# Performance work log

Measured on AMD Instinct MI355X. Metric: run time of the kernel, lower is better.

The kernel has to match this reference:

```python
import jax, jax.numpy as jnp
import numpy as np

CUT_DIST = 4.0            # cut_dist_bohr
FEATURES = 20
EPSILON = 1e-11
BOHR = 0.5291772105638411  # distance_mul (ase.units.Bohr)
POS_SCALE = 2.5


def setup_inputs() -> dict:
    key = jax.random.key(0)
    k1, k2 = jax.random.split(key)
    source = jax.random.normal(k1, (1, 4096, 3), dtype=jnp.float32) * POS_SCALE
    target = jax.random.normal(k2, (1, 2048, 3), dtype=jnp.float32) * POS_SCALE
    return {"source": source, "target": target}


def reference(source, target):
    # Pairwise diff between every source (probe) and target (atom): [B, N, M, 3]
    diff = target[:, None, :, :] - source[:, :, None, :]
    dist = jnp.sqrt(jnp.sum(diff * diff, axis=-1))            # [B, N, M]
    mask = dist < CUT_DIST                                    # [B, N, M] bool (self_send=True keeps d==0)
    direction = diff / (dist[..., None] + EPSILON)            # [B, N, M, 3]
    # sinc radial basis expansion on distances converted with distance_mul (Bohr)
    d = dist * BOHR + EPSILON                                 # [B, N, M]
    n = jnp.arange(1, FEATURES + 1, dtype=d.dtype)            # [F]
    d_exp = d[..., None]                                      # [B, N, M, 1]
    expansion = jnp.sin(n * jnp.pi * d_exp / CUT_DIST) / d_exp  # [B, N, M, F]
    return dist, direction, mask, expansion
```

## Files before the change

### kernel.cpp

```cpp
#include <hip/hip_runtime.h>
#include <math.h>

typedef float v4f __attribute__((ext_vector_type(4)));

#define CUT  4.0f
#define EPS  1e-11f
#define BOHR 0.5291772105638411f
#define PI_F 3.14159265358979323846f

#define LDS_FLOATS 18432

__device__ __forceinline__ float bperm(unsigned int lane, float v) {
    return __int_as_float(
        __builtin_amdgcn_ds_bpermute((int)(lane << 2), __float_as_int(v)));
}

__global__ __launch_bounds__(256) void deepdft_staged_kernel(
    const float* __restrict__ src,
    const float* __restrict__ tgt,
    float* __restrict__ out,
    unsigned int N, unsigned int M)
{
    __shared__ __align__(16) float lds[LDS_FLOATS];
    float* lsrc = lds;
    float* ltgt = lds + 3u * N;

    const unsigned int total = N * M;
    const unsigned int tid   = threadIdx.x;

    {
        const unsigned int ns = 3u * N;
        if ((ns & 3u) == 0u) {
            const unsigned int ns4 = ns >> 2;
            for (unsigned int i = tid; i < ns4; i += blockDim.x)
                ((v4f*)lsrc)[i] = ((const v4f*)src)[i];
        } else {
            for (unsigned int i = tid; i < ns; i += blockDim.x) lsrc[i] = src[i];
        }
        const unsigned int nt = 3u * M;
        if ((ns & 3u) == 0u && (nt & 3u) == 0u) {
            const unsigned int nt4 = nt >> 2;
            for (unsigned int i = tid; i < nt4; i += blockDim.x)
                ((v4f*)ltgt)[i] = ((const v4f*)tgt)[i];
        } else {
            for (unsigned int i = tid; i < nt; i += blockDim.x) ltgt[i] = tgt[i];
        }
    }
    __syncthreads();

    float* __restrict__ dist_o = out;
    float* __restrict__ dir_o  = out + (size_t)total;
    float* __restrict__ mask_o = out + (size_t)4 * total;
    float* __restrict__ exp_o  = out + (size_t)5 * total;

    const unsigned int lane   = tid & 63u;
    const unsigned int waves  = (gridDim.x * blockDim.x) >> 6;
    const unsigned int wtiles = (total + 63u) >> 6;

    for (unsigned int w = (blockIdx.x * blockDim.x + tid) >> 6;
         w < wtiles; w += waves) {
        const unsigned int base = w << 6;
        const unsigned int idx  = base + lane;
        const unsigned int cidx = (idx < total) ? idx : (total - 1u);

        unsigned int n = cidx / M;
        unsigned int m = cidx - n * M;

        float sx = lsrc[3u*n + 0], sy = lsrc[3u*n + 1], sz = lsrc[3u*n + 2];
        float tx = ltgt[3u*m + 0], ty = ltgt[3u*m + 1], tz = ltgt[3u*m + 2];

        float dx = tx - sx, dy = ty - sy, dz = tz - sz;
        float d2   = fmaf(dx, dx, fmaf(dy, dy, dz * dz));
        float dist = sqrtf(d2);
        float inv  = 1.0f / (dist + EPS);

        if (idx < total) {
            dist_o[idx] = dist;
            mask_o[idx] = (dist < CUT) ? 1.0f : 0.0f;
        }

        float ux = dx * inv, uy = dy * inv, uz = dz * inv;
        float d    = fmaf(dist, BOHR, EPS);
        float invd = 1.0f / d;
        float x    = (PI_F / CUT) * d;

        {
            float* gdir = dir_o + (size_t)3 * base;
            #pragma unroll
            for (int k = 0; k < 3; ++k) {
                unsigned int e = lane + 64u * (unsigned)k;
                unsigned int p = (e * 10923u) >> 15;
                unsigned int c = e - 3u * p;
                float vx = bperm(p, ux);
                float vy = bperm(p, uy);
                float vz = bperm(p, uz);
                float val = (c == 0u) ? vx : ((c == 1u) ? vy : vz);
                if (base + p < total) gdir[e] = val;
            }
        }

        {
            v4f* gexp = reinterpret_cast<v4f*>(exp_o) + (size_t)5 * base;
            #pragma unroll
            for (int k = 0; k < 5; ++k) {
                unsigned int j = lane + 64u * (unsigned)k;
                unsigned int p = (j * 6554u) >> 15;
                unsigned int g = j - 5u * p;
                float xv = bperm(p, x);
                float iv = bperm(p, invd);
                float n0 = (float)(4u * g + 1u);
                v4f v;
                v.x = __sinf( n0         * xv) * iv;
                v.y = __sinf((n0 + 1.0f) * xv) * iv;
                v.z = __sinf((n0 + 2.0f) * xv) * iv;
                v.w = __sinf((n0 + 3.0f) * xv) * iv;
                if (base + p < total) gexp[j] = v;
            }
        }
    }
}

__global__ __launch_bounds__(256) void deepdft_global_kernel(
    const float* __restrict__ src,
    const float* __restrict__ tgt,
    float* __restrict__ out,
    unsigned int N, unsigned int M)
{
    const unsigned int total = N * M;
    float* __restrict__ dist_o = out;
    float* __restrict__ dir_o  = out + (size_t)total;
    float* __restrict__ mask_o = out + (size_t)4 * total;
    float* __restrict__ exp_o  = out + (size_t)5 * total;

    const unsigned int lane   = threadIdx.x & 63u;
    const unsigned int waves  = (gridDim.x * blockDim.x) >> 6;
    const unsigned int wtiles = (total + 63u) >> 6;

    for (unsigned int w = (blockIdx.x * blockDim.x + threadIdx.x) >> 6;
         w < wtiles; w += waves) {
        const unsigned int base = w << 6;
        const unsigned int idx  = base + lane;
        const unsigned int cidx = (idx < total) ? idx : (total - 1u);
        unsigned int n = cidx / M;
        unsigned int m = cidx - n * M;

        float sx = src[3u*n + 0], sy = src[3u*n + 1], sz = src[3u*n + 2];
        float tx = tgt[3u*m + 0], ty = tgt[3u*m + 1], tz = tgt[3u*m + 2];
        float dx = tx - sx, dy = ty - sy, dz = tz - sz;
        float dist = sqrtf(fmaf(dx, dx, fmaf(dy, dy, dz * dz)));
        float inv  = 1.0f / (dist + EPS);

        if (idx < total) {
            dist_o[idx] = dist;
            mask_o[idx] = (dist < CUT) ? 1.0f : 0.0f;
        }
        float ux = dx * inv, uy = dy * inv, uz = dz * inv;
        float d    = fmaf(dist, BOHR, EPS);
        float invd = 1.0f / d;
        float x    = (PI_F / CUT) * d;

        {
            float* gdir = dir_o + (size_t)3 * base;
            #pragma unroll
            for (int k = 0; k < 3; ++k) {
                unsigned int e = lane + 64u * (unsigned)k;
                unsigned int p = (e * 10923u) >> 15;
                unsigned int c = e - 3u * p;
                float vx = bperm(p, ux);
                float vy = bperm(p, uy);
                float vz = bperm(p, uz);
                float val = (c == 0u) ? vx : ((c == 1u) ? vy : vz);
                if (base + p < total) gdir[e] = val;
            }
        }
        {
            v4f* gexp = reinterpret_cast<v4f*>(exp_o) + (size_t)5 * base;
            #pragma unroll
            for (int k = 0; k < 5; ++k) {
                unsigned int j = lane + 64u * (unsigned)k;
                unsigned int p = (j * 6554u) >> 15;
                unsigned int g = j - 5u * p;
                float xv = bperm(p, x);
                float iv = bperm(p, invd);
                float n0 = (float)(4u * g + 1u);
                v4f v;
                v.x = __sinf( n0         * xv) * iv;
                v.y = __sinf((n0 + 1.0f) * xv) * iv;
                v.z = __sinf((n0 + 2.0f) * xv) * iv;
                v.w = __sinf((n0 + 3.0f) * xv) * iv;
                if (base + p < total) gexp[j] = v;
            }
        }
    }
}

extern "C" void kernel_launch(void* const* d_in, const int* in_sizes, int n_in,
                              void* d_out, int out_size, void* d_ws, size_t ws_size,
                              hipStream_t stream) {
    const float* src = (const float*)d_in[0];
    const float* tgt = (const float*)d_in[1];
    float* out = (float*)d_out;

    unsigned int N = (unsigned int)(in_sizes[0] / 3);
    unsigned int M = (unsigned int)(in_sizes[1] / 3);
    unsigned int total = N * M;

    const unsigned int block = 256;
    unsigned int wtiles = (total + 63u) >> 6;
    unsigned int blocks = (wtiles + (block / 64) - 1) / (block / 64);
    if (blocks > 2048u) blocks = 2048u;

    if (3u * (N + M) <= (unsigned)LDS_FLOATS) {
        deepdft_staged_kernel<<<blocks, block, 0, stream>>>(src, tgt, out, N, M);
    } else {
        deepdft_global_kernel<<<blocks, block, 0, stream>>>(src, tgt, out, N, M);
    }
}
```

Measured before the change: 160.1 us.

## Batch eight wave tiles per phase with contiguous chunking and fewer blocks

The LDS-staged kernel now gives each wave a contiguous chunk of tiles instead of a grid stride. It processes tiles in groups of eight: first it computes distances for all eight and keeps the per-tile values in registers, then it writes all directions, then all expansions. The grid is capped at 512 blocks instead of 2048, so each block loads the source and target arrays into LDS fewer times in total. The aim is more independent work per wave and more back-to-back stores, at the cost of higher register pressure and fewer resident waves to hide latency.

```diff
diff --git a/kernel.cpp b/kernel.cpp
--- a/kernel.cpp
+++ b/kernel.cpp
@@ -9,13 +9,14 @@
 #define PI_F 3.14159265358979323846f
 
 #define LDS_FLOATS 18432
+#define T 8
 
 __device__ __forceinline__ float bperm(unsigned int lane, float v) {
     return __int_as_float(
         __builtin_amdgcn_ds_bpermute((int)(lane << 2), __float_as_int(v)));
 }
 
-__global__ __launch_bounds__(256) void deepdft_staged_kernel(
+__global__ __launch_bounds__(256) void deepdft_phased_kernel(
     const float* __restrict__ src,
     const float* __restrict__ tgt,
     float* __restrict__ out,
@@ -30,19 +31,15 @@
 
     {
         const unsigned int ns = 3u * N;
-        if ((ns & 3u) == 0u) {
-            const unsigned int ns4 = ns >> 2;
+        const unsigned int nt = 3u * M;
+        if ((ns & 3u) == 0u && (nt & 3u) == 0u) {
+            const unsigned int ns4 = ns >> 2, nt4 = nt >> 2;
             for (unsigned int i = tid; i < ns4; i += blockDim.x)
                 ((v4f*)lsrc)[i] = ((const v4f*)src)[i];
-        } else {
-            for (unsigned int i = tid; i < ns; i += blockDim.x) lsrc[i] = src[i];
-        }
-        const unsigned int nt = 3u * M;
-        if ((ns & 3u) == 0u && (nt & 3u) == 0u) {
-            const unsigned int nt4 = nt >> 2;
             for (unsigned int i = tid; i < nt4; i += blockDim.x)
                 ((v4f*)ltgt)[i] = ((const v4f*)tgt)[i];
         } else {
+            for (unsigned int i = tid; i < ns; i += blockDim.x) lsrc[i] = src[i];
             for (unsigned int i = tid; i < nt; i += blockDim.x) ltgt[i] = tgt[i];
         }
     }
@@ -56,29 +53,123 @@
     const unsigned int lane   = tid & 63u;
     const unsigned int waves  = (gridDim.x * blockDim.x) >> 6;
     const unsigned int wtiles = (total + 63u) >> 6;
-
-    for (unsigned int w = (blockIdx.x * blockDim.x + tid) >> 6;
+    const unsigned int wid    = (blockIdx.x * blockDim.x + tid) >> 6;
+
+    const unsigned int chunk = (wtiles + waves - 1u) / waves;
+    const unsigned int tbeg  = wid * chunk;
+    const unsigned int tend  = (tbeg + chunk < wtiles) ? (tbeg + chunk) : wtiles;
+
+    for (unsigned int c = tbeg; c < tend; c += T) {
+        const unsigned int nt = (tend - c < T) ? (tend - c) : T;
+        float rux[T], ruy[T], ruz[T], rx[T], rinv[T];
+
+        #pragma unroll
+        for (unsigned int t = 0; t < T; ++t) {
+            if (t < nt) {
+                const unsigned int base = (c + t) << 6;
+                const unsigned int idx  = base + lane;
+                const unsigned int cidx = (idx < total) ? idx : (total - 1u);
+                unsigned int n = cidx / M;
+                unsigned int m = cidx - n * M;
+
+                float sx = lsrc[3u*n + 0], sy = lsrc[3u*n + 1], sz = lsrc[3u*n + 2];
+                float tx = ltgt[3u*m + 0], ty = ltgt[3u*m + 1], tz = ltgt[3u*m + 2];
+
+                float dx = tx - sx, dy = ty - sy, dz = tz - sz;
+                float dist = sqrtf(fmaf(dx, dx, fmaf(dy, dy, dz * dz)));
+                float inv  = 1.0f / (dist + EPS);
+
+                if (idx < total) {
+                    dist_o[idx] = dist;
+                    mask_o[idx] = (dist < CUT) ? 1.0f : 0.0f;
+                }
+                rux[t] = dx * inv;
+                ruy[t] = dy * inv;
+                ruz[t] = dz * inv;
+                float d = fmaf(dist, BOHR, EPS);
+                rinv[t] = 1.0f / d;
+                rx[t]   = (PI_F / CUT) * d;
+            }
+        }
+
+        #pragma unroll
+        for (unsigned int t = 0; t < T; ++t) {
+            if (t < nt) {
+                const unsigned int base = (c + t) << 6;
+                float* gdir = dir_o + (size_t)3 * base;
+                #pragma unroll
+                for (int k = 0; k < 3; ++k) {
+                    unsigned int e = lane + 64u * (unsigned)k;
+                    unsigned int p = (e * 10923u) >> 15;
+                    unsigned int cc = e - 3u * p;
+                    float vx = bperm(p, rux[t]);
+                    float vy = bperm(p, ruy[t]);
+                    float vz = bperm(p, ruz[t]);
+                    float val = (cc == 0u) ? vx : ((cc == 1u) ? vy : vz);
+                    if (base + p < total) gdir[e] = val;
+                }
+            }
+        }
+
+        #pragma unroll
+        for (unsigned int t = 0; t < T; ++t) {
+            if (t < nt) {
+                const unsigned int base = (c + t) << 6;
+                v4f* gexp = reinterpret_cast<v4f*>(exp_o) + (size_t)5 * base;
+                #pragma unroll
+                for (int k = 0; k < 5; ++k) {
+                    unsigned int j = lane + 64u * (unsigned)k;
+                    unsigned int p = (j * 6554u) >> 15;
+                    unsigned int g = j - 5u * p;
+                    float xv = bperm(p, rx[t]);
+                    float iv = bperm(p, rinv[t]);
+                    float n0 = (float)(4u * g + 1u);
+                    v4f v;
+                    v.x = __sinf( n0         * xv) * iv;
+                    v.y = __sinf((n0 + 1.0f) * xv) * iv;
+                    v.z = __sinf((n0 + 2.0f) * xv) * iv;
+                    v.w = __sinf((n0 + 3.0f) * xv) * iv;
+                    if (base + p < total) gexp[j] = v;
+                }
+            }
+        }
+    }
+}
+
+__global__ __launch_bounds__(256) void deepdft_global_kernel(
+    const float* __restrict__ src,
+    const float* __restrict__ tgt,
+    float* __restrict__ out,
+    unsigned int N, unsigned int M)
+{
+    const unsigned int total = N * M;
+    float* __restrict__ dist_o = out;
+    float* __restrict__ dir_o  = out + (size_t)total;
+    float* __restrict__ mask_o = out + (size_t)4 * total;
+    float* __restrict__ exp_o  = out + (size_t)5 * total;
+
+    const unsigned int lane   = threadIdx.x & 63u;
+    const unsigned int waves  = (gridDim.x * blockDim.x) >> 6;
+    const unsigned int wtiles = (total + 63u) >> 6;
+
+    for (unsigned int w = (blockIdx.x * blockDim.x + threadIdx.x) >> 6;
          w < wtiles; w += waves) {
         const unsigned int base = w << 6;
         const unsigned int idx  = base + lane;
         const unsigned int cidx = (idx < total) ? idx : (total - 1u);
-
         unsigned int n = cidx / M;
         unsigned int m = cidx - n * M;
 
-        float sx = lsrc[3u*n + 0], sy = lsrc[3u*n + 1], sz = lsrc[3u*n + 2];
-        float tx = ltgt[3u*m + 0], ty = ltgt[3u*m + 1], tz = ltgt[3u*m + 2];
-
+        float sx = src[3u*n + 0], sy = src[3u*n + 1], sz = src[3u*n + 2];
+        float tx = tgt[3u*m + 0], ty = tgt[3u*m + 1], tz = tgt[3u*m + 2];
         float dx = tx - sx, dy = ty - sy, dz = tz - sz;
-        float d2   = fmaf(dx, dx, fmaf(dy, dy, dz * dz));
-        float dist = sqrtf(d2);
+        float dist = sqrtf(fmaf(dx, dx, fmaf(dy, dy, dz * dz)));
         float inv  = 1.0f / (dist + EPS);
 
         if (idx < total) {
             dist_o[idx] = dist;
             mask_o[idx] = (dist < CUT) ? 1.0f : 0.0f;
         }
-
         float ux = dx * inv, uy = dy * inv, uz = dz * inv;
         float d    = fmaf(dist, BOHR, EPS);
         float invd = 1.0f / d;
@@ -90,15 +181,14 @@
             for (int k = 0; k < 3; ++k) {
                 unsigned int e = lane + 64u * (unsigned)k;
                 unsigned int p = (e * 10923u) >> 15;
-                unsigned int c = e - 3u * p;
+                unsigned int cc = e - 3u * p;
                 float vx = bperm(p, ux);
                 float vy = bperm(p, uy);
                 float vz = bperm(p, uz);
-                float val = (c == 0u) ? vx : ((c == 1u) ? vy : vz);
+                float val = (cc == 0u) ? vx : ((cc == 1u) ? vy : vz);
                 if (base + p < total) gdir[e] = val;
             }
         }
-
         {
             v4f* gexp = reinterpret_cast<v4f*>(exp_o) + (size_t)5 * base;
             #pragma unroll
@@ -120,80 +210,6 @@
     }
 }
 
-__global__ __launch_bounds__(256) void deepdft_global_kernel(
-    const float* __restrict__ src,
-    const float* __restrict__ tgt,
-    float* __restrict__ out,
-    unsigned int N, unsigned int M)
-{
-    const unsigned int total = N * M;
-    float* __restrict__ dist_o = out;
-    float* __restrict__ dir_o  = out + (size_t)total;
-    float* __restrict__ mask_o = out + (size_t)4 * total;
-    float* __restrict__ exp_o  = out + (size_t)5 * total;
-
-    const unsigned int lane   = threadIdx.x & 63u;
-    const unsigned int waves  = (gridDim.x * blockDim.x) >> 6;
-    const unsigned int wtiles = (total + 63u) >> 6;
-
-    for (unsigned int w = (blockIdx.x * blockDim.x + threadIdx.x) >> 6;
-         w < wtiles; w += waves) {
-        const unsigned int base = w << 6;
-        const unsigned int idx  = base + lane;
-        const unsigned int cidx = (idx < total) ? idx : (total - 1u);
-        unsigned int n = cidx / M;
-        unsigned int m = cidx - n * M;
-
-        float sx = src[3u*n + 0], sy = src[3u*n + 1], sz = src[3u*n + 2];
-        float tx = tgt[3u*m + 0], ty = tgt[3u*m + 1], tz = tgt[3u*m + 2];
-        float dx = tx - sx, dy = ty - sy, dz = tz - sz;
-        float dist = sqrtf(fmaf(dx, dx, fmaf(dy, dy, dz * dz)));
-        float inv  = 1.0f / (dist + EPS);
-
-        if (idx < total) {
-            dist_o[idx] = dist;
-            mask_o[idx] = (dist < CUT) ? 1.0f : 0.0f;
-        }
-        float ux = dx * inv, uy = dy * inv, uz = dz * inv;
-        float d    = fmaf(dist, BOHR, EPS);
-        float invd = 1.0f / d;
-        float x    = (PI_F / CUT) * d;
-
-        {
-            float* gdir = dir_o + (size_t)3 * base;
-            #pragma unroll
-            for (int k = 0; k < 3; ++k) {
-                unsigned int e = lane + 64u * (unsigned)k;
-                unsigned int p = (e * 10923u) >> 15;
-                unsigned int c = e - 3u * p;
-                float vx = bperm(p, ux);
-                float vy = bperm(p, uy);
-                float vz = bperm(p, uz);
-                float val = (c == 0u) ? vx : ((c == 1u) ? vy : vz);
-                if (base + p < total) gdir[e] = val;
-            }
-        }
-        {
-            v4f* gexp = reinterpret_cast<v4f*>(exp_o) + (size_t)5 * base;
-            #pragma unroll
-            for (int k = 0; k < 5; ++k) {
-                unsigned int j = lane + 64u * (unsigned)k;
-                unsigned int p = (j * 6554u) >> 15;
-                unsigned int g = j - 5u * p;
-                float xv = bperm(p, x);
-                float iv = bperm(p, invd);
-                float n0 = (float)(4u * g + 1u);
-                v4f v;
-                v.x = __sinf( n0         * xv) * iv;
-                v.y = __sinf((n0 + 1.0f) * xv) * iv;
-                v.z = __sinf((n0 + 2.0f) * xv) * iv;
-                v.w = __sinf((n0 + 3.0f) * xv) * iv;
-                if (base + p < total) gexp[j] = v;
-            }
-        }
-    }
-}
-
 extern "C" void kernel_launch(void* const* d_in, const int* in_sizes, int n_in,
                               void* d_out, int out_size, void* d_ws, size_t ws_size,
                               hipStream_t stream) {
@@ -204,15 +220,15 @@
     unsigned int N = (unsigned int)(in_sizes[0] / 3);
     unsigned int M = (unsigned int)(in_sizes[1] / 3);
     unsigned int total = N * M;
-
-    const unsigned int block = 256;
     unsigned int wtiles = (total + 63u) >> 6;
-    unsigned int blocks = (wtiles + (block / 64) - 1) / (block / 64);
-    if (blocks > 2048u) blocks = 2048u;
 
     if (3u * (N + M) <= (unsigned)LDS_FLOATS) {
-        deepdft_staged_kernel<<<blocks, block, 0, stream>>>(src, tgt, out, N, M);
+        unsigned int blocks = (wtiles + 3u) / 4u;
+        if (blocks > 512u) blocks = 512u;
+        deepdft_phased_kernel<<<blocks, 256, 0, stream>>>(src, tgt, out, N, M);
     } else {
-        deepdft_global_kernel<<<blocks, block, 0, stream>>>(src, tgt, out, N, M);
-    }
-}
+        unsigned int blocks = (wtiles + 3u) / 4u;
+        if (blocks > 2048u) blocks = 2048u;
+        deepdft_global_kernel<<<blocks, 256, 0, stream>>>(src, tgt, out, N, M);
+    }
+}
```

Result: slower. 175.9 us (+9.8%).
